# Kernel optimization log

Measured on AMD Instinct MI355X. Metric: run time of the kernel, lower is better.

Reference implementation:

```python
import jax, jax.numpy as jnp
import numpy as np

B, T, D, KDIM = 256, 512, 256, 256

def setup_inputs() -> dict:
    key = jax.random.key(0)
    k1, k2, k3 = jax.random.split(key, 3)
    inputs = jax.random.normal(k1, (B, T, D), dtype=jnp.float32)
    # glorot-style scaling for stability of the recurrence
    U = jax.random.normal(k2, (D, KDIM), dtype=jnp.float32) * (1.0 / np.sqrt(D))
    W = jax.random.normal(k3, (KDIM, KDIM), dtype=jnp.float32) * (1.0 / np.sqrt(KDIM))
    b = jnp.zeros((KDIM,), dtype=jnp.float32)
    return {"inputs": inputs, "U": U, "W": W, "b": b}

def reference(inputs, U, W, b):
    # vanilla RNN: h_t = tanh(x_t U + h_{t-1} W + b); returns final hidden state
    xU = jnp.einsum('btd,dk->btk', inputs, U) + b  # precompute input projection [B,T,K]

    def step(h, xu_t):
        h = jnp.tanh(xu_t + h @ W)
        return h, None

    h0 = jnp.zeros((inputs.shape[0], W.shape[0]), dtype=inputs.dtype)
    h_final, _ = jax.lax.scan(step, h0, jnp.swapaxes(xU, 0, 1))  # scan over time
    # original keras code keeps a singleton time axis on the state: [B,1,K]
    return h_final[:, None, :]
```

## Files before the change

### kernel.cpp

```cpp
#include <hip/hip_runtime.h>
#include <hip/hip_bf16.h>


typedef _Float16 half8_t __attribute__((ext_vector_type(8)));
typedef _Float16 half2_t __attribute__((ext_vector_type(2)));
typedef float    float4_t __attribute__((ext_vector_type(4)));

#define MFMA16(a, b, c) __builtin_amdgcn_mfma_f32_16x16x32_f16((a), (b), (c), 0, 0, 0)

__device__ __forceinline__ half2_t pk_h2(float a, float b) {
    auto r = __builtin_amdgcn_cvt_pkrtz(a, b);
    return __builtin_bit_cast(half2_t, r);
}

__device__ __forceinline__ float fast_tanh(float x) {
    float e = __expf(2.0f * x);
    return 1.0f - 2.0f * __builtin_amdgcn_rcpf(e + 1.0f);
}

__global__ void transpose_u(const float* __restrict__ U, _Float16* __restrict__ Ut) {
    int id = blockIdx.x * 256 + threadIdx.x;
    int d = id >> 8, n = id & 255;
    Ut[n * 264 + d] = (_Float16)U[id];
}

__global__ __launch_bounds__(256, 2) void xu_gemm(
    const float* __restrict__ x,
    const _Float16* __restrict__ Ut,
    half2_t* __restrict__ xu)
{
    __shared__ char lds[61440];
    const int tid = threadIdx.x;
    const int lane = tid & 63, w = tid >> 6, l15 = lane & 15, q = lane >> 4;
    const int bx = blockIdx.x;
    const int t_blk = bx >> 1;
    const int b0 = (bx & 1) * 128;

    float4 ar[4];
    uint4  br[4];

    auto loadA = [&](int it) {
#pragma unroll
        for (int i = 0; i < 4; ++i) {
            int u = tid + 256 * i, row = u >> 3, seg = u & 7;
            ar[i] = *(const float4*)(x + ((size_t)(b0 + row) * 512 + t_blk) * 256
                                       + it * 32 + seg * 4);
        }
    };
    auto loadB = [&](int it) {
#pragma unroll
        for (int i = 0; i < 4; ++i) {
            int u = tid + 256 * i, p = u >> 2, seg = u & 3;
            int c = 32 * (p >> 5) + 2 * (p & 15) + ((p >> 4) & 1);
            br[i] = *(const uint4*)((const char*)Ut + c * 528 + it * 64 + seg * 16);
        }
    };
    auto writeAB = [&](int s) {
        char* As = lds + s * 10240;
        char* Bs = lds + 20480 + s * 20480;
#pragma unroll
        for (int i = 0; i < 4; ++i) {
            int u = tid + 256 * i, row = u >> 3, seg = u & 7;
            half2_t p0 = pk_h2(ar[i].x, ar[i].y);
            half2_t p1 = pk_h2(ar[i].z, ar[i].w);
            uint2 v;
            v.x = __builtin_bit_cast(unsigned, p0);
            v.y = __builtin_bit_cast(unsigned, p1);
            *(uint2*)(As + row * 80 + seg * 8) = v;
        }
#pragma unroll
        for (int i = 0; i < 4; ++i) {
            int u = tid + 256 * i, p = u >> 2, seg = u & 3;
            *(uint4*)(Bs + p * 80 + seg * 16) = br[i];
        }
    };

    float4_t acc[32];
#pragma unroll
    for (int i = 0; i < 32; ++i) { acc[i][0] = 0.f; acc[i][1] = 0.f; acc[i][2] = 0.f; acc[i][3] = 0.f; }

    loadA(0); loadB(0); writeAB(0);
    __syncthreads();

    for (int it = 0; it < 8; ++it) {
        if (it < 7) { loadA(it + 1); loadB(it + 1); }
        const char* As = lds + (it & 1) * 10240;
        const char* Bs = lds + 20480 + (it & 1) * 20480;
        half8_t af[2];
#pragma unroll
        for (int ms = 0; ms < 2; ++ms)
            af[ms] = *(const half8_t*)(As + (32 * w + 16 * ms + l15) * 80 + q * 16);
#pragma unroll
        for (int ns = 0; ns < 16; ++ns) {
            half8_t bf = *(const half8_t*)(Bs + (16 * ns + l15) * 80 + q * 16);
            acc[ns * 2 + 0] = MFMA16(af[0], bf, acc[ns * 2 + 0]);
            acc[ns * 2 + 1] = MFMA16(af[1], bf, acc[ns * 2 + 1]);
        }
        if (it < 7) writeAB((it + 1) & 1);
        __syncthreads();
    }

#pragma unroll
    for (int ms = 0; ms < 2; ++ms)
#pragma unroll
        for (int j = 0; j < 8; ++j)
#pragma unroll
            for (int i = 0; i < 4; ++i) {
                float v0 = acc[(2 * j) * 2 + ms][i];
                float v1 = acc[(2 * j + 1) * 2 + ms][i];
                half2_t p = pk_h2(v0, v1);
                int m_g = bx * 128 + 32 * w + 16 * ms + q * 4 + i;
                int c = 32 * j + 2 * l15;
                xu[(size_t)m_g * 128 + (c >> 1)] = p;
            }
}

__global__ __launch_bounds__(512, 2) void rnn_scan(
    const half2_t* __restrict__ xu,
    const float* __restrict__ W,
    const float* __restrict__ bias,
    float* __restrict__ out)
{
    __shared__ char lds[16896];
    const int tid = threadIdx.x;
    const int lane = tid & 63, w = tid >> 6, l15 = lane & 15, q = lane >> 4;
    const int blk = blockIdx.x;
    const int c0 = 32 * w + 2 * l15;

    half8_t wf[2][8];
#pragma unroll
    for (int tt = 0; tt < 2; ++tt)
#pragma unroll
        for (int c = 0; c < 8; ++c) {
            half8_t f;
#pragma unroll
            for (int j = 0; j < 8; ++j) {
                int k = 32 * c + q * 8 + j;
                f[j] = (_Float16)W[k * 256 + c0 + tt];
            }
            wf[tt][c] = f;
        }
    const float b0 = bias[c0], b1 = bias[c0 + 1];

    for (int i = tid; i < 16896 / 4; i += 512) ((int*)lds)[i] = 0;

    const int rowg0 = 16 * blk + q * 4;
    half2_t xu_n[4];
    {
        int xb = (0 * 256 + rowg0) * 128 + (c0 >> 1);
#pragma unroll
        for (int i = 0; i < 4; ++i) xu_n[i] = xu[xb + i * 128];
    }
    __syncthreads();

    char* const hbuf0 = (char*)lds;
    char* const hbuf1 = (char*)lds + 8448;

    for (int t = 0; t < 512; ++t) {
        float4_t acc0, acc1;
#pragma unroll
        for (int i = 0; i < 4; ++i) { acc0[i] = (float)xu_n[i][0]; acc1[i] = (float)xu_n[i][1]; }

        int tn = (t < 511) ? (t + 1) : 511;
        int xb = (tn * 256 + rowg0) * 128 + (c0 >> 1);
#pragma unroll
        for (int i = 0; i < 4; ++i) xu_n[i] = xu[xb + i * 128];

        const char* hcur = (t & 1) ? hbuf1 : hbuf0;
        half8_t af[8];
#pragma unroll
        for (int c = 0; c < 8; ++c)
            af[c] = *(const half8_t*)(hcur + l15 * 528 + c * 64 + q * 16);

#pragma unroll
        for (int c = 0; c < 8; ++c) {
            acc0 = MFMA16(af[c], wf[0][c], acc0);
            acc1 = MFMA16(af[c], wf[1][c], acc1);
        }

        if (t == 511) {
#pragma unroll
            for (int i = 0; i < 4; ++i) {
                float v0 = fast_tanh(acc0[i] + b0);
                float v1 = fast_tanh(acc1[i] + b1);
                float2 st; st.x = v0; st.y = v1;
                *(float2*)(&out[(rowg0 + i) * 256 + c0]) = st;
            }
        } else {
            char* hnext = ((t + 1) & 1) ? hbuf1 : hbuf0;
#pragma unroll
            for (int i = 0; i < 4; ++i) {
                float v0 = fast_tanh(acc0[i] + b0);
                float v1 = fast_tanh(acc1[i] + b1);
                half2_t p = pk_h2(v0, v1);
                *(half2_t*)(hnext + (q * 4 + i) * 528 + c0 * 2) = p;
            }
        }
        __syncthreads();
    }
}

extern "C" void kernel_launch(void* const* d_in, const int* in_sizes, int n_in,
                              void* d_out, int out_size, void* d_ws, size_t ws_size,
                              hipStream_t stream) {
    const float* x = (const float*)d_in[0];
    const float* U = (const float*)d_in[1];
    const float* W = (const float*)d_in[2];
    const float* b = (const float*)d_in[3];
    float* out = (float*)d_out;

    char* ws = (char*)d_ws;
    _Float16* Ut = (_Float16*)ws;
    half2_t*  xu = (half2_t*)(ws + 262144);

    transpose_u<<<256, 256, 0, stream>>>(U, Ut);
    xu_gemm<<<1024, 256, 0, stream>>>(x, Ut, xu);
    rnn_scan<<<16, 512, 0, stream>>>(xu, W, b, out);
}
```

Before: 543.2 us.

## Halve scan block to four waves, swizzle LDS state, prefetch xu two steps ahead

The recurrent scan now runs with 256 threads (4 waves) per block instead of 512, and each wave computes two 32-column slices. This halves the participants in the per-step barrier and doubles the MFMA work per wave. The hidden-state LDS buffer drops its padding in favour of an XOR swizzle to avoid bank conflicts, and xu is prefetched two timesteps ahead with two register sets. The input GEMM now assigns blocks by (batch, 128-timestep chunk) while keeping the time-major xu layout. The trade-off is more registers per wave and longer serial MFMA chains in each step.

```diff
diff --git a/kernel.cpp b/kernel.cpp
--- a/kernel.cpp
+++ b/kernel.cpp
@@ -33,8 +33,8 @@
     const int tid = threadIdx.x;
     const int lane = tid & 63, w = tid >> 6, l15 = lane & 15, q = lane >> 4;
     const int bx = blockIdx.x;
-    const int t_blk = bx >> 1;
-    const int b0 = (bx & 1) * 128;
+    const int b_idx = bx >> 2;
+    const int t0 = (bx & 3) * 128;
 
     float4 ar[4];
     uint4  br[4];
@@ -43,7 +43,7 @@
 #pragma unroll
         for (int i = 0; i < 4; ++i) {
             int u = tid + 256 * i, row = u >> 3, seg = u & 7;
-            ar[i] = *(const float4*)(x + ((size_t)(b0 + row) * 512 + t_blk) * 256
+            ar[i] = *(const float4*)(x + ((size_t)b_idx * 512 + t0 + row) * 256
                                        + it * 32 + seg * 4);
         }
     };
@@ -109,94 +109,131 @@
                 float v0 = acc[(2 * j) * 2 + ms][i];
                 float v1 = acc[(2 * j + 1) * 2 + ms][i];
                 half2_t p = pk_h2(v0, v1);
-                int m_g = bx * 128 + 32 * w + 16 * ms + q * 4 + i;
+                int t_g = t0 + 32 * w + 16 * ms + q * 4 + i;
                 int c = 32 * j + 2 * l15;
-                xu[(size_t)m_g * 128 + (c >> 1)] = p;
+                xu[((size_t)t_g * 256 + b_idx) * 128 + (c >> 1)] = p;
             }
 }
 
-__global__ __launch_bounds__(512, 2) void rnn_scan(
+__global__ __launch_bounds__(256, 1) void rnn_scan(
     const half2_t* __restrict__ xu,
     const float* __restrict__ W,
     const float* __restrict__ bias,
     float* __restrict__ out)
 {
-    __shared__ char lds[16896];
+    __shared__ char lds[16384];
     const int tid = threadIdx.x;
     const int lane = tid & 63, w = tid >> 6, l15 = lane & 15, q = lane >> 4;
     const int blk = blockIdx.x;
-    const int c0 = 32 * w + 2 * l15;
-
-    half8_t wf[2][8];
-#pragma unroll
-    for (int tt = 0; tt < 2; ++tt)
-#pragma unroll
-        for (int c = 0; c < 8; ++c) {
-            half8_t f;
-#pragma unroll
-            for (int j = 0; j < 8; ++j) {
-                int k = 32 * c + q * 8 + j;
-                f[j] = (_Float16)W[k * 256 + c0 + tt];
+
+    half8_t wf[2][2][8];
+#pragma unroll
+    for (int s = 0; s < 2; ++s)
+#pragma unroll
+        for (int tt = 0; tt < 2; ++tt)
+#pragma unroll
+            for (int c = 0; c < 8; ++c) {
+                half8_t f;
+#pragma unroll
+                for (int j = 0; j < 8; ++j) {
+                    int k = 32 * c + q * 8 + j;
+                    f[j] = (_Float16)W[k * 256 + 64 * w + 32 * s + 2 * l15 + tt];
+                }
+                wf[s][tt][c] = f;
             }
-            wf[tt][c] = f;
-        }
-    const float b0 = bias[c0], b1 = bias[c0 + 1];
-
-    for (int i = tid; i < 16896 / 4; i += 512) ((int*)lds)[i] = 0;
-
-    const int rowg0 = 16 * blk + q * 4;
-    half2_t xu_n[4];
-    {
-        int xb = (0 * 256 + rowg0) * 128 + (c0 >> 1);
-#pragma unroll
-        for (int i = 0; i < 4; ++i) xu_n[i] = xu[xb + i * 128];
-    }
+    float bs[2][2];
+#pragma unroll
+    for (int s = 0; s < 2; ++s)
+#pragma unroll
+        for (int tt = 0; tt < 2; ++tt)
+            bs[s][tt] = bias[64 * w + 32 * s + 2 * l15 + tt];
+
+    for (int i = tid; i < 4096; i += 256) ((int*)lds)[i] = 0;
+
+    int raddr[8];
+#pragma unroll
+    for (int c = 0; c < 8; ++c)
+        raddr[c] = l15 * 512 + 16 * ((4 * c + q) ^ (l15 & 7));
+    int waddr[2][4];
+#pragma unroll
+    for (int s = 0; s < 2; ++s)
+#pragma unroll
+        for (int i = 0; i < 4; ++i) {
+            int r = 4 * q + i;
+            int g = 8 * w + 4 * s + (l15 >> 2);
+            waddr[s][i] = r * 512 + (g ^ (r & 7)) * 16 + (l15 & 3) * 4;
+        }
+
+    const int rowg0 = 16 * blk + 4 * q;
+    const int cpair0 = 32 * w + l15;
+
+    auto load_xu = [&](half2_t (&dst)[8], int t) {
+#pragma unroll
+        for (int s = 0; s < 2; ++s)
+#pragma unroll
+            for (int i = 0; i < 4; ++i)
+                dst[s * 4 + i] = xu[((size_t)t * 256 + rowg0 + i) * 128 + cpair0 + 16 * s];
+    };
+
+    half2_t xc[8], xn[8];
+    load_xu(xc, 0);
+    load_xu(xn, 1);
     __syncthreads();
 
-    char* const hbuf0 = (char*)lds;
-    char* const hbuf1 = (char*)lds + 8448;
-
-    for (int t = 0; t < 512; ++t) {
-        float4_t acc0, acc1;
-#pragma unroll
-        for (int i = 0; i < 4; ++i) { acc0[i] = (float)xu_n[i][0]; acc1[i] = (float)xu_n[i][1]; }
-
-        int tn = (t < 511) ? (t + 1) : 511;
-        int xb = (tn * 256 + rowg0) * 128 + (c0 >> 1);
-#pragma unroll
-        for (int i = 0; i < 4; ++i) xu_n[i] = xu[xb + i * 128];
-
-        const char* hcur = (t & 1) ? hbuf1 : hbuf0;
+    auto step = [&](half2_t (&xreg)[8], int t) {
+        float4_t acc[2][2];
+#pragma unroll
+        for (int s = 0; s < 2; ++s)
+#pragma unroll
+            for (int tt = 0; tt < 2; ++tt)
+#pragma unroll
+                for (int i = 0; i < 4; ++i)
+                    acc[s][tt][i] = (float)xreg[s * 4 + i][tt];
+
+        int tp = t + 2 > 511 ? 511 : t + 2;
+        load_xu(xreg, tp);
+
+        const char* base = lds + (t & 1) * 8192;
         half8_t af[8];
 #pragma unroll
         for (int c = 0; c < 8; ++c)
-            af[c] = *(const half8_t*)(hcur + l15 * 528 + c * 64 + q * 16);
-
-#pragma unroll
-        for (int c = 0; c < 8; ++c) {
-            acc0 = MFMA16(af[c], wf[0][c], acc0);
-            acc1 = MFMA16(af[c], wf[1][c], acc1);
-        }
+            af[c] = *(const half8_t*)(base + raddr[c]);
+
+#pragma unroll
+        for (int c = 0; c < 8; ++c)
+#pragma unroll
+            for (int s = 0; s < 2; ++s)
+#pragma unroll
+                for (int tt = 0; tt < 2; ++tt)
+                    acc[s][tt] = MFMA16(af[c], wf[s][tt][c], acc[s][tt]);
 
         if (t == 511) {
 #pragma unroll
-            for (int i = 0; i < 4; ++i) {
-                float v0 = fast_tanh(acc0[i] + b0);
-                float v1 = fast_tanh(acc1[i] + b1);
-                float2 st; st.x = v0; st.y = v1;
-                *(float2*)(&out[(rowg0 + i) * 256 + c0]) = st;
-            }
+            for (int s = 0; s < 2; ++s)
+#pragma unroll
+                for (int i = 0; i < 4; ++i) {
+                    float v0 = fast_tanh(acc[s][0][i] + bs[s][0]);
+                    float v1 = fast_tanh(acc[s][1][i] + bs[s][1]);
+                    float2 st; st.x = v0; st.y = v1;
+                    *(float2*)(&out[(rowg0 + i) * 256 + 64 * w + 32 * s + 2 * l15]) = st;
+                }
         } else {
-            char* hnext = ((t + 1) & 1) ? hbuf1 : hbuf0;
-#pragma unroll
-            for (int i = 0; i < 4; ++i) {
-                float v0 = fast_tanh(acc0[i] + b0);
-                float v1 = fast_tanh(acc1[i] + b1);
-                half2_t p = pk_h2(v0, v1);
-                *(half2_t*)(hnext + (q * 4 + i) * 528 + c0 * 2) = p;
-            }
+            char* nb = lds + ((t + 1) & 1) * 8192;
+#pragma unroll
+            for (int s = 0; s < 2; ++s)
+#pragma unroll
+                for (int i = 0; i < 4; ++i) {
+                    float v0 = fast_tanh(acc[s][0][i] + bs[s][0]);
+                    float v1 = fast_tanh(acc[s][1][i] + bs[s][1]);
+                    *(half2_t*)(nb + waddr[s][i]) = pk_h2(v0, v1);
+                }
         }
         __syncthreads();
+    };
+
+    for (int t2 = 0; t2 < 512; t2 += 2) {
+        step(xc, t2);
+        step(xn, t2 + 1);
     }
 }
 
@@ -215,5 +252,5 @@
 
     transpose_u<<<256, 256, 0, stream>>>(U, Ut);
     xu_gemm<<<1024, 256, 0, stream>>>(x, Ut, xu);
-    rnn_scan<<<16, 512, 0, stream>>>(xu, W, b, out);
-}
+    rnn_scan<<<16, 256, 0, stream>>>(xu, W, b, out);
+}
```

After: 650.6 us. +19.8%, slower.
